# Kernel tuning notes

Measured on AMD Instinct MI355X. Metric: run time of the kernel, lower is better.

Reference implementation:

```python
import jax, jax.numpy as jnp
import numpy as np

N, D, C = 4096, 1024, 1000
EPS = 1e-8


def _remove_diag(M):
    # faithful to torch M[off_diag_mask].view(h, h-1) via strided-reshape trick
    h = M.shape[0]
    return M.reshape(-1)[1:].reshape(h - 1, h + 1)[:, :-1].reshape(h, h - 1)


def _cosine_sim_matrix(x, y):
    # torch CosineSimilarity: x.y / max(||x||*||y||, eps)
    xn = jnp.linalg.norm(x, axis=-1, keepdims=True)
    yn = jnp.linalg.norm(y, axis=-1, keepdims=True)
    num = jnp.einsum('id,jd->ij', x, y)
    den = jnp.maximum(xn * yn.T, EPS)
    return num / den


def setup_inputs() -> dict:
    key = jax.random.key(0)
    k1, k2, k3, k4 = jax.random.split(key, 4)
    return {
        'inst_embed': jax.random.normal(k1, (N, D), dtype=jnp.float32),
        'anchor': jax.random.normal(k2, (N, D), dtype=jnp.float32),
        'cls_mask': jax.random.randint(k3, (C, N), 0, 2, dtype=jnp.int32),
        'labels': jax.random.randint(k4, (N,), 0, C, dtype=jnp.int64),
        'temperature': jnp.float32(1.0),
    }


def reference(inst_embed, anchor, cls_mask, labels, temperature):
    # augmentation=None branch of Conditional_Embedding_Contrastive_loss.forward
    sim = _cosine_sim_matrix(inst_embed, inst_embed)          # [N,N]
    instance_zone = jnp.exp(_remove_diag(sim) / temperature)  # [N,N-1]
    mask_neg = _remove_diag(cls_mask[labels].astype(instance_zone.dtype))  # [N,N-1]
    inst2inst_pos = instance_zone * mask_neg
    # elementwise cosine sim between inst_embed and anchor rows
    dot = jnp.sum(inst_embed * anchor, axis=-1)
    nrm = jnp.maximum(jnp.linalg.norm(inst_embed, axis=-1) * jnp.linalg.norm(anchor, axis=-1), EPS)
    inst2embed_pos = jnp.exp((dot / nrm) / temperature)       # [N]
    numerator = inst2inst_pos.sum(axis=1) + inst2embed_pos
    denominator = inst2embed_pos + instance_zone.sum(axis=1)
    return -jnp.mean(jnp.log(numerator / denominator))
```

## Files before the change

### kernel.cpp

```cpp
#include <hip/hip_runtime.h>
#include <hip/hip_bf16.h>
#include <math.h>


#define NN   4096
#define DD   1024
#define NCLS 1000
#define EPSF 1e-8f
#define MW   (NN / 32)
#define NTILE 528
#define SLOTS 32

typedef short bf16x8 __attribute__((ext_vector_type(8)));
typedef float f32x4  __attribute__((ext_vector_type(4)));

__global__ __launch_bounds__(256) void k_pack(const int* __restrict__ cmask,
                                              const int* __restrict__ lraw,
                                              unsigned int* __restrict__ mbits,
                                              int* __restrict__ lab) {
  const int b = blockIdx.x;
  if (b < NCLS * MW / 256) {
    const int wword = b * 256 + threadIdx.x;
    const int* src = cmask + (size_t)wword * 32;
    unsigned int v = 0;
    #pragma unroll
    for (int q = 0; q < 8; ++q) {
      const int4 c = *(const int4*)(src + q * 4);
      v |= (c.x != 0 ? 1u : 0u) << (q * 4 + 0);
      v |= (c.y != 0 ? 1u : 0u) << (q * 4 + 1);
      v |= (c.z != 0 ? 1u : 0u) << (q * 4 + 2);
      v |= (c.w != 0 ? 1u : 0u) << (q * 4 + 3);
    }
    mbits[wword] = v;
  } else {
    __shared__ int stride_s;
    if (threadIdx.x == 0) {
      int stride = 2;
      #pragma unroll
      for (int t = 0; t < 8; ++t) {
        int lo = lraw[2 * t], hi = lraw[2 * t + 1];
        if (hi != 0 || (unsigned)lo >= (unsigned)NCLS) { stride = 1; break; }
      }
      stride_s = stride;
    }
    __syncthreads();
    const int i = (b - NCLS * MW / 256) * 256 + threadIdx.x;
    lab[i] = lraw[i * stride_s];
  }
}

__global__ __launch_bounds__(256) void k_rowstats(
    const float* __restrict__ X, const float* __restrict__ A,
    const float* __restrict__ Tp, ushort* __restrict__ Xb,
    float* __restrict__ rnx, float* __restrict__ rnT,
    float* __restrict__ epos, float* __restrict__ out) {
  const int i = blockIdx.x;
  const int t = threadIdx.x;
  const size_t base = (size_t)i * DD + t * 4;
  const float4 xv = *(const float4*)(X + base);
  const float4 av = *(const float4*)(A + base);
  float sxx = xv.x * xv.x + xv.y * xv.y + xv.z * xv.z + xv.w * xv.w;
  float saa = av.x * av.x + av.y * av.y + av.z * av.z + av.w * av.w;
  float sxa = xv.x * av.x + xv.y * av.y + xv.z * av.z + xv.w * av.w;

  ushort4 pk;
  { __hip_bfloat16 b;
    b = __float2bfloat16(xv.x); pk.x = *(const ushort*)&b;
    b = __float2bfloat16(xv.y); pk.y = *(const ushort*)&b;
    b = __float2bfloat16(xv.z); pk.z = *(const ushort*)&b;
    b = __float2bfloat16(xv.w); pk.w = *(const ushort*)&b; }
  *(ushort4*)(Xb + base) = pk;

  #pragma unroll
  for (int off = 32; off > 0; off >>= 1) {
    sxx += __shfl_down(sxx, off);
    saa += __shfl_down(saa, off);
    sxa += __shfl_down(sxa, off);
  }
  __shared__ float red[3][4];
  const int w = t >> 6;
  if ((t & 63) == 0) { red[0][w] = sxx; red[1][w] = saa; red[2][w] = sxa; }
  __syncthreads();
  if (t == 0) {
    const float a  = red[0][0] + red[0][1] + red[0][2] + red[0][3];
    const float bb = red[1][0] + red[1][1] + red[1][2] + red[1][3];
    const float c  = red[2][0] + red[2][1] + red[2][2] + red[2][3];
    const float nxi = sqrtf(a), nai = sqrtf(bb);
    const float rT  = 1.0f / Tp[0];
    const float r   = 1.0f / fmaxf(nxi, 1e-20f);
    rnx[i] = r;
    rnT[i] = r * rT;
    epos[i] = expf((c / fmaxf(nxi * nai, EPSF)) * rT);
    if (i == 0) out[0] = 0.f;
  }
}

#define BM 128
#define BK 64

__global__ __launch_bounds__(256) void k_gram(
    const ushort* __restrict__ Xb, const float* __restrict__ rnx,
    const float* __restrict__ rnT,
    const int* __restrict__ lab, const unsigned int* __restrict__ mbits,
    float* __restrict__ scrF, float* __restrict__ scrM) {
  __shared__ __align__(16) char As[BM * BK * 2];
  __shared__ __align__(16) char Bs[BM * BK * 2];
  const int tid  = threadIdx.x;
  const int lane = tid & 63;
  const int w    = tid >> 6;
  const int wr   = w >> 1, wc = w & 1;

  const int t = blockIdx.x;
  int a = (int)((sqrtf(8.f * (float)t + 1.f) - 1.f) * 0.5f);
  while ((a + 1) * (a + 2) / 2 <= t) ++a;
  while (a * (a + 1) / 2 > t) --a;
  const int by = t - a * (a + 1) / 2;
  const int bx = a;
  const bool offdiag = (bx != by);
  const int i0 = by * BM;
  const int j0 = bx * BM;

  const int sslot = (lane & 7) ^ (lane >> 3);

  f32x4 acc[4][4];
  #pragma unroll
  for (int m = 0; m < 4; ++m)
    #pragma unroll
    for (int n = 0; n < 4; ++n)
      acc[m][n] = (f32x4){0.f, 0.f, 0.f, 0.f};

  const ushort* pA[4];
  const ushort* pB[4];
  #pragma unroll
  for (int q = 0; q < 4; ++q) {
    const int row = q * 32 + w * 8 + (lane >> 3);
    pA[q] = Xb + (size_t)(i0 + row) * DD + sslot * 8;
    pB[q] = Xb + (size_t)(j0 + row) * DD + sslot * 8;
  }

  for (int k0 = 0; k0 < DD; k0 += BK) {
    #pragma unroll
    for (int q = 0; q < 4; ++q) {
      __builtin_amdgcn_global_load_lds(
          (const __attribute__((address_space(1))) void*)(pA[q] + k0),
          (__attribute__((address_space(3))) void*)(As + (q * 4 + w) * 1024), 16, 0, 0);
      __builtin_amdgcn_global_load_lds(
          (const __attribute__((address_space(1))) void*)(pB[q] + k0),
          (__attribute__((address_space(3))) void*)(Bs + (q * 4 + w) * 1024), 16, 0, 0);
    }
    __syncthreads();

    #pragma unroll
    for (int ks = 0; ks < 2; ++ks) {
      const int slot = ((ks << 2) + (lane >> 4)) ^ (lane & 7);
      bf16x8 af[4], bfr[4];
      #pragma unroll
      for (int m = 0; m < 4; ++m) {
        const int r = (wr << 6) + (m << 4) + (lane & 15);
        af[m] = *(const bf16x8*)(As + r * 128 + (slot << 4));
      }
      #pragma unroll
      for (int n = 0; n < 4; ++n) {
        const int r = (wc << 6) + (n << 4) + (lane & 15);
        bfr[n] = *(const bf16x8*)(Bs + r * 128 + (slot << 4));
      }
      #pragma unroll
      for (int m = 0; m < 4; ++m)
        #pragma unroll
        for (int n = 0; n < 4; ++n)
          acc[m][n] = __builtin_amdgcn_mfma_f32_16x16x32_bf16(af[m], bfr[n], acc[m][n], 0, 0, 0);
    }
    __syncthreads();
  }

  float* LF = (float*)As;
  float* LM = LF + 256;
  float* GF = LM + 256;
  float* GM = GF + 256;

  float rnT_j[4];
  unsigned long long wj[4];
  #pragma unroll
  for (int n = 0; n < 4; ++n) {
    const int j = j0 + (wc << 6) + (n << 4) + (lane & 15);
    rnT_j[n] = rnT[j];
    wj[n] = *(const unsigned long long*)(mbits + (size_t)lab[j] * MW + (i0 >> 5) + (wr << 1));
  }
  float pse[4] = {0.f, 0.f, 0.f, 0.f}, psm[4] = {0.f, 0.f, 0.f, 0.f};

  #pragma unroll
  for (int m = 0; m < 4; ++m) {
    #pragma unroll
    for (int r = 0; r < 4; ++r) {
      const int irow = (m << 4) + ((lane >> 4) << 2) + r;
      const int i = i0 + (wr << 6) + irow;
      const float rni = rnx[i];
      const unsigned long long wi =
          *(const unsigned long long*)(mbits + (size_t)lab[i] * MW + (j0 >> 5) + (wc << 1));
      float se = 0.f, sm = 0.f;
      #pragma unroll
      for (int n = 0; n < 4; ++n) {
        const int j = j0 + (wc << 6) + (n << 4) + (lane & 15);
        float e = __expf(acc[m][n][r] * rni * rnT_j[n]);
        if (i == j) e = 0.f;
        se += e;
        const int bposj = (n << 4) + (lane & 15);
        sm += ((wi >> bposj) & 1ull) ? e : 0.f;
        pse[n] += e;
        psm[n] += ((wj[n] >> irow) & 1ull) ? e : 0.f;
      }
      #pragma unroll
      for (int off = 1; off < 16; off <<= 1) {
        se += __shfl_xor(se, off);
        sm += __shfl_xor(sm, off);
      }
      if ((lane & 15) == 0) {
        LF[(wc << 7) + (wr << 6) + irow] = se;
        LM[(wc << 7) + (wr << 6) + irow] = sm;
      }
    }
  }
  if (offdiag) {
    #pragma unroll
    for (int n = 0; n < 4; ++n) {
      float se = pse[n], sm = psm[n];
      se += __shfl_xor(se, 16); se += __shfl_xor(se, 32);
      sm += __shfl_xor(sm, 16); sm += __shfl_xor(sm, 32);
      if (lane < 16) {
        GF[(wr << 7) + (wc << 6) + (n << 4) + lane] = se;
        GM[(wr << 7) + (wc << 6) + (n << 4) + lane] = sm;
      }
    }
  }
  __syncthreads();

  if (tid < 128) {
    scrF[(size_t)bx * NN + i0 + tid] = LF[tid] + LF[128 + tid];
    if (offdiag) scrF[(size_t)by * NN + j0 + tid] = GF[tid] + GF[128 + tid];
  } else {
    const int u = tid - 128;
    scrM[(size_t)bx * NN + i0 + u] = LM[u] + LM[128 + u];
    if (offdiag) scrM[(size_t)by * NN + j0 + u] = GM[u] + GM[128 + u];
  }
}

__global__ __launch_bounds__(256) void k_final(
    const float* __restrict__ scrF, const float* __restrict__ scrM,
    const float* __restrict__ epos, float* __restrict__ out) {
  const int idx = blockIdx.x * 256 + threadIdx.x;
  float sf = 0.f, sm = 0.f;
  #pragma unroll
  for (int s = 0; s < SLOTS; ++s) {
    sf += scrF[(size_t)s * NN + idx];
    sm += scrM[(size_t)s * NN + idx];
  }
  const float ep  = epos[idx];
  const float num = sm + ep;
  const float den = ep + sf;
  float v = (logf(den) - logf(num)) * (1.0f / (float)NN);
  #pragma unroll
  for (int off = 32; off > 0; off >>= 1) v += __shfl_down(v, off);
  __shared__ float red[4];
  if ((threadIdx.x & 63) == 0) red[threadIdx.x >> 6] = v;
  __syncthreads();
  if (threadIdx.x == 0) atomicAdd(out, red[0] + red[1] + red[2] + red[3]);
}

extern "C" void kernel_launch(void* const* d_in, const int* in_sizes, int n_in,
                              void* d_out, int out_size, void* d_ws, size_t ws_size,
                              hipStream_t stream) {
  const float* X     = (const float*)d_in[0];
  const float* A     = (const float*)d_in[1];
  const int*   cmask = (const int*)d_in[2];
  const int*   lraw  = (const int*)d_in[3];
  const float* Tp    = (const float*)d_in[4];
  float* out = (float*)d_out;

  char* ws = (char*)d_ws;
  ushort* Xb   = (ushort*)ws;
  float* rnx   = (float*)(ws + (size_t)NN * DD * 2);
  float* rnT   = rnx + NN;
  float* epos  = rnT + NN;
  int*   lab   = (int*)(epos + NN);
  unsigned int* mbits = (unsigned int*)(lab + NN);
  float* scrF  = (float*)(mbits + (size_t)NCLS * MW);
  float* scrM  = scrF + (size_t)SLOTS * NN;

  hipLaunchKernelGGL(k_pack,     dim3(NCLS * MW / 256 + NN / 256), dim3(256), 0, stream, cmask, lraw, mbits, lab);
  hipLaunchKernelGGL(k_rowstats, dim3(NN),    dim3(256), 0, stream, X, A, Tp, Xb, rnx, rnT, epos, out);
  hipLaunchKernelGGL(k_gram,     dim3(NTILE), dim3(256), 0, stream, Xb, rnx, rnT, lab, mbits, scrF, scrM);
  hipLaunchKernelGGL(k_final,    dim3(NN/256), dim3(256), 0, stream, scrF, scrM, epos, out);
}
```

Measured before the change: 86.01 us.

## Double-buffer LDS tiles in gram kernel to prefetch next K-step

```diff
diff --git a/kernel.cpp b/kernel.cpp
--- a/kernel.cpp
+++ b/kernel.cpp
@@ -97,14 +97,15 @@
 
 #define BM 128
 #define BK 64
+#define NSTEP (DD / BK)
 
 __global__ __launch_bounds__(256) void k_gram(
     const ushort* __restrict__ Xb, const float* __restrict__ rnx,
     const float* __restrict__ rnT,
     const int* __restrict__ lab, const unsigned int* __restrict__ mbits,
     float* __restrict__ scrF, float* __restrict__ scrM) {
-  __shared__ __align__(16) char As[BM * BK * 2];
-  __shared__ __align__(16) char Bs[BM * BK * 2];
+  __shared__ __align__(16) char As[2][BM * BK * 2];
+  __shared__ __align__(16) char Bs[2][BM * BK * 2];
   const int tid  = threadIdx.x;
   const int lane = tid & 63;
   const int w    = tid >> 6;
@@ -138,18 +139,31 @@
     pB[q] = Xb + (size_t)(j0 + row) * DD + sslot * 8;
   }
 
-  for (int k0 = 0; k0 < DD; k0 += BK) {
-    #pragma unroll
-    for (int q = 0; q < 4; ++q) {
-      __builtin_amdgcn_global_load_lds(
-          (const __attribute__((address_space(1))) void*)(pA[q] + k0),
-          (__attribute__((address_space(3))) void*)(As + (q * 4 + w) * 1024), 16, 0, 0);
-      __builtin_amdgcn_global_load_lds(
-          (const __attribute__((address_space(1))) void*)(pB[q] + k0),
-          (__attribute__((address_space(3))) void*)(Bs + (q * 4 + w) * 1024), 16, 0, 0);
-    }
-    __syncthreads();
-
+  #pragma unroll
+  for (int q = 0; q < 4; ++q) {
+    __builtin_amdgcn_global_load_lds(
+        (const __attribute__((address_space(1))) void*)(pA[q]),
+        (__attribute__((address_space(3))) void*)(As[0] + (q * 4 + w) * 1024), 16, 0, 0);
+    __builtin_amdgcn_global_load_lds(
+        (const __attribute__((address_space(1))) void*)(pB[q]),
+        (__attribute__((address_space(3))) void*)(Bs[0] + (q * 4 + w) * 1024), 16, 0, 0);
+  }
+  __syncthreads();
+
+  int cur = 0;
+  for (int s = 0; s < NSTEP; ++s) {
+    if (s + 1 < NSTEP) {
+      const int k0 = (s + 1) * BK;
+      #pragma unroll
+      for (int q = 0; q < 4; ++q) {
+        __builtin_amdgcn_global_load_lds(
+            (const __attribute__((address_space(1))) void*)(pA[q] + k0),
+            (__attribute__((address_space(3))) void*)(As[cur ^ 1] + (q * 4 + w) * 1024), 16, 0, 0);
+        __builtin_amdgcn_global_load_lds(
+            (const __attribute__((address_space(1))) void*)(pB[q] + k0),
+            (__attribute__((address_space(3))) void*)(Bs[cur ^ 1] + (q * 4 + w) * 1024), 16, 0, 0);
+      }
+    }
     #pragma unroll
     for (int ks = 0; ks < 2; ++ks) {
       const int slot = ((ks << 2) + (lane >> 4)) ^ (lane & 7);
@@ -157,12 +171,12 @@
       #pragma unroll
       for (int m = 0; m < 4; ++m) {
         const int r = (wr << 6) + (m << 4) + (lane & 15);
-        af[m] = *(const bf16x8*)(As + r * 128 + (slot << 4));
+        af[m] = *(const bf16x8*)(As[cur] + r * 128 + (slot << 4));
       }
       #pragma unroll
       for (int n = 0; n < 4; ++n) {
         const int r = (wc << 6) + (n << 4) + (lane & 15);
-        bfr[n] = *(const bf16x8*)(Bs + r * 128 + (slot << 4));
+        bfr[n] = *(const bf16x8*)(Bs[cur] + r * 128 + (slot << 4));
       }
       #pragma unroll
       for (int m = 0; m < 4; ++m)
@@ -171,9 +185,10 @@
           acc[m][n] = __builtin_amdgcn_mfma_f32_16x16x32_bf16(af[m], bfr[n], acc[m][n], 0, 0, 0);
     }
     __syncthreads();
-  }
-
-  float* LF = (float*)As;
+    cur ^= 1;
+  }
+
+  float* LF = (float*)As[0];
   float* LM = LF + 256;
   float* GF = LM + 256;
   float* GM = GF + 256;
```

After: 88.62 us. 3.0% more time.
